# Optimization experiments

Measured on AMD Instinct MI355X. Metric: run time of the kernel, lower is better.

Reference implementation:

```python
import jax, jax.numpy as jnp
import numpy as np

H = 16
D_MODEL = 1024
D_K = D_MODEL // H


def setup_inputs() -> dict:
    key = jax.random.key(0)
    ks = jax.random.split(key, 12)
    B, S = 2, 2048
    scale = 1.0 / np.sqrt(D_MODEL)
    inp = {
        "query": jax.random.normal(ks[0], (B, S, D_MODEL), jnp.float32),
        "key": jax.random.normal(ks[1], (B, S, D_MODEL), jnp.float32),
        "value": jax.random.normal(ks[2], (B, S, D_MODEL), jnp.float32),
        "mask": jax.random.randint(ks[3], (B, S, S), 0, 2, jnp.int32),
        "w_q": jax.random.normal(ks[4], (D_MODEL, D_MODEL), jnp.float32) * scale,
        "b_q": jnp.zeros((D_MODEL,), jnp.float32),
        "w_k": jax.random.normal(ks[5], (D_MODEL, D_MODEL), jnp.float32) * scale,
        "b_k": jnp.zeros((D_MODEL,), jnp.float32),
        "w_v": jax.random.normal(ks[6], (D_MODEL, D_MODEL), jnp.float32) * scale,
        "b_v": jnp.zeros((D_MODEL,), jnp.float32),
        "w_o": jax.random.normal(ks[7], (D_MODEL, D_MODEL), jnp.float32) * scale,
        "b_o": jnp.zeros((D_MODEL,), jnp.float32),
    }
    return inp


def reference(query, key, value, mask, w_q, b_q, w_k, b_k, w_v, b_v, w_o, b_o):
    B, S, _ = query.shape
    # linear projections (torch nn.Linear: x @ W^T + b)
    q = query @ w_q.T + b_q
    k = key @ w_k.T + b_k
    v = value @ w_v.T + b_v
    # split heads -> [B, H, S, D_K]
    q = q.reshape(B, S, H, D_K).transpose(0, 2, 1, 3)
    k = k.reshape(B, S, H, D_K).transpose(0, 2, 1, 3)
    v = v.reshape(B, S, H, D_K).transpose(0, 2, 1, 3)
    # scores [B, H, S, S]; original masks BEFORE dividing by sqrt(d_k)
    scores = jnp.einsum("bhqd,bhkd->bhqk", q, k)
    m = mask[:, None, :, :]  # broadcast over heads (mask.unsqueeze(1))
    scores = jnp.where(m == 0, jnp.float32(-1e9), scores)
    scores = scores / jnp.sqrt(jnp.float32(D_K))
    attn = jax.nn.softmax(scores, axis=-1)
    # dropout is identity in eval mode
    ctx = jnp.einsum("bhqk,bhkd->bhqd", attn, v)
    ctx = ctx.transpose(0, 2, 1, 3).reshape(B, S, H * D_K)
    return ctx @ w_o.T + b_o
```

## Files before the change

kernel.cpp:

```cpp
#include <hip/hip_runtime.h>
#include <hip/hip_bf16.h>
#include <stdint.h>

typedef __attribute__((ext_vector_type(8))) short short8;
typedef __attribute__((ext_vector_type(4))) short short4v;
typedef __attribute__((ext_vector_type(4))) float f32x4;
typedef __attribute__((ext_vector_type(4))) unsigned short us4;
typedef unsigned short ushort_t;

#define LDS_AS __attribute__((address_space(3)))
#define GLB_AS __attribute__((address_space(1)))

__device__ __forceinline__ void gload_lds16(const void* g, void* l) {
    __builtin_amdgcn_global_load_lds((const GLB_AS uint32_t*)g, (LDS_AS uint32_t*)l, 16, 0, 0);
}

__device__ __forceinline__ unsigned short f2bf(float f) {
    union { float f; uint32_t u; } v; v.f = f;
    uint32_t r = v.u + 0x7FFFu + ((v.u >> 16) & 1u);
    return (unsigned short)(r >> 16);
}

__device__ __forceinline__ float fexp2(float x) {
#if __has_builtin(__builtin_amdgcn_exp2f)
    return __builtin_amdgcn_exp2f(x);
#else
    return exp2f(x);
#endif
}

__device__ __forceinline__ uint32_t fbits(float f) {
    union { float f; uint32_t u; } v; v.f = f; return v.u;
}

__device__ __forceinline__ f32x4 mfma32(short8 a, short8 b, f32x4 c) {
    return __builtin_amdgcn_mfma_f32_16x16x32_bf16(a, b, c, 0, 0, 0);
}
__device__ __forceinline__ f32x4 mfma16(short4v a, short4v b, f32x4 c) {
    return __builtin_amdgcn_mfma_f32_16x16x16bf16_1k(a, b, c, 0, 0, 0);
}

__device__ __forceinline__ short8 lds_frag(const char* base, int row, int kc) {
    int byte = row * 128 + ((kc ^ (row & 7)) << 4);
    return *(const short8*)(base + byte);
}

__global__ __launch_bounds__(256) void cvt_all(
    const float* p0, const float* p1, const float* p2, const float* p3,
    const float* p4, const float* p5, const float* p6,
    ushort_t* o0, ushort_t* o1, ushort_t* o2, ushort_t* o3,
    ushort_t* o4, ushort_t* o5, ushort_t* o6) {
    int z = blockIdx.y;
    const float* in = z == 0 ? p0 : z == 1 ? p1 : z == 2 ? p2 : z == 3 ? p3 : z == 4 ? p4 : z == 5 ? p5 : p6;
    ushort_t* out = z == 0 ? o0 : z == 1 ? o1 : z == 2 ? o2 : z == 3 ? o3 : z == 4 ? o4 : z == 5 ? o5 : o6;
    int n4 = z < 3 ? 1048576 : 262144;
    int i = blockIdx.x * 256 + threadIdx.x;
    int stride = gridDim.x * 256;
    for (; i < n4; i += stride) {
        float4 f = ((const float4*)in)[i];
        us4 o;
        o[0] = f2bf(f.x); o[1] = f2bf(f.y); o[2] = f2bf(f.z); o[3] = f2bf(f.w);
        ((us4*)out)[i] = o;
    }
}

__global__ __launch_bounds__(256) void pack_mask(const int* __restrict__ mask,
                                                 unsigned long long* __restrict__ out) {
    int i = blockIdx.x * 256 + threadIdx.x;
    unsigned long long bits = __ballot(mask[i] != 0);
    if ((threadIdx.x & 63) == 0) {
        int k = i & 2047, q = (i >> 11) & 2047, b = i >> 22;
        out[((size_t)b * 32 + (k >> 6)) * 2048 + q] = bits;
    }
}

template<int MI>
__device__ __forceinline__ void gemm_core(const ushort_t* Ab, const ushort_t* Wb,
                                          char* ldsA, char* ldsW, int tid, f32x4 acc[MI][4]) {
    constexpr int K = 1024;
    int lane = tid & 63, wid = tid >> 6;
    int cl = lane & 15, gr = lane >> 4;
    int wm = (wid >> 1) * (MI * 16), wn = (wid & 1) * 64;
#pragma unroll
    for (int i = 0; i < MI; ++i)
#pragma unroll
        for (int j = 0; j < 4; ++j) acc[i][j] = (f32x4)0.0f;

    for (int kt = 0; kt < K / 64; ++kt) {
        int k0 = kt * 64;
#pragma unroll
        for (int iss = 0; iss < MI; ++iss) {
            int c = iss * 256 + tid;
            int r = c >> 3, kc = (c & 7) ^ (r & 7);
            gload_lds16(Ab + (size_t)r * K + k0 + kc * 8, ldsA + c * 16);
        }
#pragma unroll
        for (int iss = 0; iss < 4; ++iss) {
            int c = iss * 256 + tid;
            int r = c >> 3, kc = (c & 7) ^ (r & 7);
            gload_lds16(Wb + (size_t)r * K + k0 + kc * 8, ldsW + c * 16);
        }
        __syncthreads();
#pragma unroll
        for (int ks = 0; ks < 2; ++ks) {
            short8 af[MI], wf[4];
#pragma unroll
            for (int t = 0; t < MI; ++t)
                af[t] = lds_frag(ldsA, wm + t * 16 + cl, ks * 4 + gr);
#pragma unroll
            for (int t = 0; t < 4; ++t)
                wf[t] = lds_frag(ldsW, wn + t * 16 + cl, ks * 4 + gr);
#pragma unroll
            for (int i = 0; i < MI; ++i)
#pragma unroll
                for (int j = 0; j < 4; ++j)
                    acc[i][j] = mfma32(af[i], wf[j], acc[i][j]);
        }
        __syncthreads();
    }
}

template<int MI>
__global__ __launch_bounds__(256, 4)
void gemm3(const ushort_t* A0, const ushort_t* A1, const ushort_t* A2,
           const ushort_t* W0, const ushort_t* W1, const ushort_t* W2,
           const float* B0, const float* B1, const float* B2,
           void* O0, void* O1, void* O2, int mode_ovr, float scl0) {
    __shared__ char lds[MI * 4096 + 16384];
    char* ldsA = lds;
    char* ldsW = lds + MI * 4096;

    int gx = gridDim.x, gy = gridDim.y;
    int nwg = gx * gy * gridDim.z;
    int bid = blockIdx.x + gx * (blockIdx.y + gy * blockIdx.z);
    int nb = (bid & 7) * (nwg >> 3) + (bid >> 3);
    int bx = nb % gx;
    int t2 = nb / gx;
    int by = t2 % gy;
    int z = t2 / gy;

    const ushort_t* A = z == 0 ? A0 : z == 1 ? A1 : A2;
    const ushort_t* W = z == 0 ? W0 : z == 1 ? W1 : W2;
    const float* bias = z == 0 ? B0 : z == 1 ? B1 : B2;
    void* out = z == 0 ? O0 : z == 1 ? O1 : O2;
    int mode = mode_ovr >= 0 ? mode_ovr : (z == 2 ? 1 : 0);
    float scl = z == 0 ? scl0 : 1.0f;

    int tid = threadIdx.x, lane = tid & 63, wid = tid >> 6;
    int cl = lane & 15, gr = lane >> 4;
    int wm = (wid >> 1) * (MI * 16), wn = (wid & 1) * 64;
    int bm = by * (MI * 32), bn = bx * 128;

    f32x4 acc[MI][4];
    gemm_core<MI>(A + (size_t)bm * 1024, W + (size_t)bn * 1024, ldsA, ldsW, tid, acc);

#pragma unroll
    for (int j = 0; j < 4; ++j) {
        int n = bn + wn + j * 16 + cl;
        float bv = bias[n];
#pragma unroll
        for (int i = 0; i < MI; ++i) {
            int mbase = bm + wm + i * 16 + gr * 4;
            if (mode == 0) {
#pragma unroll
                for (int r = 0; r < 4; ++r) {
                    int m = mbase + r;
                    float v = (acc[i][j][r] + bv) * scl;
                    size_t idx = (((size_t)((m >> 11) * 16 + (n >> 6))) * 2048 + (m & 2047)) * 64 + (n & 63);
                    ((ushort_t*)out)[idx] = f2bf(v);
                }
            } else if (mode == 1) {
                us4 pk;
#pragma unroll
                for (int r = 0; r < 4; ++r) pk[r] = f2bf(acc[i][j][r] + bv);
                size_t idx = (((size_t)((mbase >> 11) * 16 + (n >> 6))) * 64 + (n & 63)) * 2048 + (mbase & 2047);
                *(us4*)((ushort_t*)out + idx) = pk;
            } else {
#pragma unroll
                for (int r = 0; r < 4; ++r)
                    ((float*)out)[(size_t)(mbase + r) * 1024 + n] = acc[i][j][r] + bv;
            }
        }
    }
}

__global__ __launch_bounds__(512, 4)
void attn(const ushort_t* __restrict__ Q, const ushort_t* __restrict__ Kh,
          const ushort_t* __restrict__ Vt, const unsigned long long* __restrict__ PM,
          ushort_t* __restrict__ ctx) {
    constexpr int S = 2048;
    __shared__ char lds[65536];
    int tid = threadIdx.x, lane = tid & 63, wid = tid >> 6;
    int cl = lane & 15, gr = lane >> 4, c7 = cl & 7;
    int h2 = wid & 1;
    int qg = wid >> 1;

    int blk = (blockIdx.x & 7) * 64 + (blockIdx.x >> 3);
    int bh = blk >> 4, qt = blk & 15;
    int b = bh >> 4, h = bh & 15;
    const ushort_t* Qb = Q + (size_t)bh * S * 64;
    const ushort_t* Kb = Kh + (size_t)bh * S * 64;
    const ushort_t* Vb = Vt + (size_t)bh * 64 * S;
    int q0w = qt * 128 + qg * 32;

    short8 qreg[2][2];
#pragma unroll
    for (int qf = 0; qf < 2; ++qf)
#pragma unroll
        for (int ks = 0; ks < 2; ++ks)
            qreg[qf][ks] = *(const short8*)(Qb + (size_t)(q0w + qf * 16 + cl) * 64 + ks * 32 + gr * 8);

    f32x4 acc[2][4];
    f32x4 accl[2];
#pragma unroll
    for (int qf = 0; qf < 2; ++qf) {
        accl[qf] = (f32x4)0.0f;
#pragma unroll
        for (int df = 0; df < 4; ++df) acc[qf][df] = (f32x4)0.0f;
    }

    int hs = tid >> 8, stid = tid & 255;
    int kOff[2], vOff[2], dstL[2];
#pragma unroll
    for (int iss = 0; iss < 2; ++iss) {
        int L = iss * 256 + stid;
        int r = L >> 3, c = (L & 7) ^ (r & 7);
        kOff[iss] = r * 64 + c * 8;
        vOff[iss] = r * S + c * 8;
        dstL[iss] = L * 16;
    }
    char* sbase = lds + hs * 32768;

    int aK0 = cl * 128 + ((0 * 4 + gr) ^ c7) * 16;
    int aK1 = cl * 128 + ((1 * 4 + gr) ^ c7) * 16;
    int aV[4];
#pragma unroll
    for (int nf = 0; nf < 4; ++nf)
        aV[nf] = cl * 128 + (((2 * nf) + (gr >> 1)) ^ c7) * 16 + (gr & 1) * 8;

    const unsigned long long* pmq = PM + (size_t)b * 32 * 2048 + q0w + cl;

    short4v ones;
#pragma unroll
    for (int r = 0; r < 4; ++r) ones[r] = (short)0x3F80;

    auto stage = [&](int T, int parity) {
        const ushort_t* Ks = Kb + (size_t)T * 4096;
        const ushort_t* Vs = Vb + (size_t)T * 64;
        char* dst = sbase + parity * 16384;
#pragma unroll
        for (int iss = 0; iss < 2; ++iss) {
            gload_lds16(Ks + kOff[iss], dst + dstL[iss]);
            gload_lds16(Vs + vOff[iss], dst + 8192 + dstL[iss]);
        }
    };

    stage(hs * 16, 0);
    __syncthreads();

    char* mybase = lds + h2 * 32768;
    for (int t = 0; t < 16; ++t) {
        char* cb = mybase + (t & 1) * 16384;
        if (t < 15) stage(hs * 16 + t + 1, (t + 1) & 1);

        int kvi = h2 * 16 + t;
        unsigned long long w0 = pmq[(size_t)kvi * 2048];
        unsigned long long w1 = pmq[(size_t)kvi * 2048 + 16];

        f32x4 sc[2][4];
#pragma unroll
        for (int nf = 0; nf < 4; ++nf) {
            short8 k0 = *(const short8*)(cb + aK0 + nf * 2048);
            short8 k1 = *(const short8*)(cb + aK1 + nf * 2048);
#pragma unroll
            for (int qf = 0; qf < 2; ++qf) {
                f32x4 s = mfma32(k0, qreg[qf][0], (f32x4)0.0f);
                sc[qf][nf] = mfma32(k1, qreg[qf][1], s);
            }
        }

        short4v pk[2][4];
#pragma unroll
        for (int qf = 0; qf < 2; ++qf) {
            unsigned long long ws = (qf == 0 ? w0 : w1) >> (gr * 4);
            uint32_t lo = (uint32_t)ws, hi = (uint32_t)(ws >> 32);
#pragma unroll
            for (int nf = 0; nf < 4; ++nf) {
                uint32_t wb = nf < 2 ? lo : hi;
                uint32_t u[4];
#pragma unroll
                for (int r = 0; r < 4; ++r) {
                    uint32_t bit = wb & (1u << ((nf & 1) * 16 + r));
                    float sel = bit ? sc[qf][nf][r] : -1.0e9f;
                    u[r] = fbits(fexp2(sel)) + 0x8000u;
                }
                union { uint32_t d[2]; short4v v; } pp;
                pp.d[0] = __builtin_amdgcn_perm(u[1], u[0], 0x07060302u);
                pp.d[1] = __builtin_amdgcn_perm(u[3], u[2], 0x07060302u);
                pk[qf][nf] = pp.v;
            }
        }

#pragma unroll
        for (int nf = 0; nf < 4; ++nf) {
#pragma unroll
            for (int df = 0; df < 4; ++df) {
                short4v vf = *(const short4v*)(cb + 8192 + aV[nf] + df * 2048);
                acc[0][df] = mfma16(pk[0][nf], vf, acc[0][df]);
                acc[1][df] = mfma16(pk[1][nf], vf, acc[1][df]);
            }
            accl[0] = mfma16(pk[0][nf], ones, accl[0]);
            accl[1] = mfma16(pk[1][nf], ones, accl[1]);
        }
        __syncthreads();
    }

    if (h2) {
        float* dst = (float*)(lds + qg * 10240 + lane * 160);
#pragma unroll
        for (int qf = 0; qf < 2; ++qf) {
#pragma unroll
            for (int df = 0; df < 4; ++df)
                *(f32x4*)(dst + qf * 16 + df * 4) = acc[qf][df];
            *(f32x4*)(dst + 32 + qf * 4) = accl[qf];
        }
    }
    __syncthreads();
    if (!h2) {
        const float* src = (const float*)(lds + qg * 10240 + lane * 160);
#pragma unroll
        for (int qf = 0; qf < 2; ++qf) {
#pragma unroll
            for (int df = 0; df < 4; ++df)
                acc[qf][df] += *(const f32x4*)(src + qf * 16 + df * 4);
            accl[qf] += *(const f32x4*)(src + 32 + qf * 4);
        }
#pragma unroll
        for (int qf = 0; qf < 2; ++qf) {
            float inv[4];
#pragma unroll
            for (int r = 0; r < 4; ++r) inv[r] = 1.0f / accl[qf][r];
#pragma unroll
            for (int df = 0; df < 4; ++df)
#pragma unroll
                for (int r = 0; r < 4; ++r) {
                    int q = q0w + qf * 16 + gr * 4 + r;
                    int d = df * 16 + cl;
                    ctx[((size_t)b * S + q) * 1024 + h * 64 + d] = f2bf(acc[qf][df][r] * inv[r]);
                }
        }
    }
}

extern "C" void kernel_launch(void* const* d_in, const int* in_sizes, int n_in,
                              void* d_out, int out_size, void* d_ws, size_t ws_size,
                              hipStream_t stream) {
    const float* query = (const float*)d_in[0];
    const float* key   = (const float*)d_in[1];
    const float* value = (const float*)d_in[2];
    const int*   mask  = (const int*)d_in[3];
    const float* w_q = (const float*)d_in[4];
    const float* b_q = (const float*)d_in[5];
    const float* w_k = (const float*)d_in[6];
    const float* b_k = (const float*)d_in[7];
    const float* w_v = (const float*)d_in[8];
    const float* b_v = (const float*)d_in[9];
    const float* w_o = (const float*)d_in[10];
    const float* b_o = (const float*)d_in[11];

    char* ws = (char*)d_ws;
    const size_t MB = 1 << 20;
    ushort_t* xq  = (ushort_t*)(ws + 0 * MB);
    ushort_t* xk  = (ushort_t*)(ws + 8 * MB);
    ushort_t* xv  = (ushort_t*)(ws + 16 * MB);
    ushort_t* wq  = (ushort_t*)(ws + 24 * MB);
    ushort_t* wk  = (ushort_t*)(ws + 26 * MB);
    ushort_t* wv  = (ushort_t*)(ws + 28 * MB);
    ushort_t* wo  = (ushort_t*)(ws + 30 * MB);
    ushort_t* qhm = (ushort_t*)(ws + 32 * MB);
    ushort_t* khm = (ushort_t*)(ws + 40 * MB);
    ushort_t* vt  = (ushort_t*)(ws + 48 * MB);
    unsigned long long* pm = (unsigned long long*)(ws + 56 * MB);
    ushort_t* ctx = (ushort_t*)(ws + 0 * MB);

    const float QSCALE = 0.125f * 1.44269504088896f;

    cvt_all<<<dim3(1024, 7), 256, 0, stream>>>(query, key, value, w_q, w_k, w_v, w_o,
                                               xq, xk, xv, wq, wk, wv, wo);
    pack_mask<<<32768, 256, 0, stream>>>(mask, pm);

    gemm3<2><<<dim3(8, 64, 3), 256, 0, stream>>>(xq, xk, xv, wq, wk, wv, b_q, b_k, b_v,
                                                 qhm, khm, vt, -1, QSCALE);

    attn<<<512, 512, 0, stream>>>(qhm, khm, vt, pm, ctx);

    gemm3<2><<<dim3(8, 64, 1), 256, 0, stream>>>(ctx, ctx, ctx, wo, wo, wo, b_o, b_o, b_o,
                                                 d_out, d_out, d_out, 2, 1.0f);
}
```

Before: 150.3 us.

## Double-buffer LDS tiles in projection GEMM to overlap loads with MFMA

The projection GEMM core now keeps two LDS tile buffers. It issues the async global-to-LDS loads for the next K-slice before running MFMAs on the current one, which removes the barrier that used to sit between load and compute in every iteration. Per-thread load offsets are precomputed once outside the loop. LDS use doubles, and the launch-bounds occupancy hint drops from 4 to 3 blocks per CU, so fewer waves are resident to hide latency.

```diff
diff --git a/kernel.cpp b/kernel.cpp
--- a/kernel.cpp
+++ b/kernel.cpp
@@ -76,8 +76,10 @@
 
 template<int MI>
 __device__ __forceinline__ void gemm_core(const ushort_t* Ab, const ushort_t* Wb,
-                                          char* ldsA, char* ldsW, int tid, f32x4 acc[MI][4]) {
+                                          char* lds, int tid, f32x4 acc[MI][4]) {
     constexpr int K = 1024;
+    constexpr int ABYTES = MI * 4096;
+    constexpr int TILE = ABYTES + 16384;
     int lane = tid & 63, wid = tid >> 6;
     int cl = lane & 15, gr = lane >> 4;
     int wm = (wid >> 1) * (MI * 16), wn = (wid & 1) * 64;
@@ -86,30 +88,49 @@
 #pragma unroll
         for (int j = 0; j < 4; ++j) acc[i][j] = (f32x4)0.0f;
 
+    int aOff[MI], aDst[MI], bOff[4], bDst[4];
+#pragma unroll
+    for (int iss = 0; iss < MI; ++iss) {
+        int c = iss * 256 + tid;
+        int r = c >> 3, kc = (c & 7) ^ (r & 7);
+        aOff[iss] = r * K + kc * 8;
+        aDst[iss] = c * 16;
+    }
+#pragma unroll
+    for (int iss = 0; iss < 4; ++iss) {
+        int c = iss * 256 + tid;
+        int r = c >> 3, kc = (c & 7) ^ (r & 7);
+        bOff[iss] = r * K + kc * 8;
+        bDst[iss] = c * 16;
+    }
+
+    auto stage = [&](int kt, char* dst) {
+        int k0 = kt * 64;
+#pragma unroll
+        for (int iss = 0; iss < MI; ++iss)
+            gload_lds16(Ab + aOff[iss] + k0, dst + aDst[iss]);
+#pragma unroll
+        for (int iss = 0; iss < 4; ++iss)
+            gload_lds16(Wb + bOff[iss] + k0, dst + ABYTES + bDst[iss]);
+    };
+
+    stage(0, lds);
+    __syncthreads();
+
     for (int kt = 0; kt < K / 64; ++kt) {
-        int k0 = kt * 64;
-#pragma unroll
-        for (int iss = 0; iss < MI; ++iss) {
-            int c = iss * 256 + tid;
-            int r = c >> 3, kc = (c & 7) ^ (r & 7);
-            gload_lds16(Ab + (size_t)r * K + k0 + kc * 8, ldsA + c * 16);
-        }
-#pragma unroll
-        for (int iss = 0; iss < 4; ++iss) {
-            int c = iss * 256 + tid;
-            int r = c >> 3, kc = (c & 7) ^ (r & 7);
-            gload_lds16(Wb + (size_t)r * K + k0 + kc * 8, ldsW + c * 16);
-        }
-        __syncthreads();
+        char* cb = lds + (kt & 1) * TILE;
+        if (kt < K / 64 - 1) stage(kt + 1, lds + ((kt + 1) & 1) * TILE);
+        char* cA = cb;
+        char* cW = cb + ABYTES;
 #pragma unroll
         for (int ks = 0; ks < 2; ++ks) {
             short8 af[MI], wf[4];
 #pragma unroll
             for (int t = 0; t < MI; ++t)
-                af[t] = lds_frag(ldsA, wm + t * 16 + cl, ks * 4 + gr);
+                af[t] = lds_frag(cA, wm + t * 16 + cl, ks * 4 + gr);
 #pragma unroll
             for (int t = 0; t < 4; ++t)
-                wf[t] = lds_frag(ldsW, wn + t * 16 + cl, ks * 4 + gr);
+                wf[t] = lds_frag(cW, wn + t * 16 + cl, ks * 4 + gr);
 #pragma unroll
             for (int i = 0; i < MI; ++i)
 #pragma unroll
@@ -121,14 +142,12 @@
 }
 
 template<int MI>
-__global__ __launch_bounds__(256, 4)
+__global__ __launch_bounds__(256, 3)
 void gemm3(const ushort_t* A0, const ushort_t* A1, const ushort_t* A2,
            const ushort_t* W0, const ushort_t* W1, const ushort_t* W2,
            const float* B0, const float* B1, const float* B2,
            void* O0, void* O1, void* O2, int mode_ovr, float scl0) {
-    __shared__ char lds[MI * 4096 + 16384];
-    char* ldsA = lds;
-    char* ldsW = lds + MI * 4096;
+    __shared__ char lds[2 * (MI * 4096 + 16384)];
 
     int gx = gridDim.x, gy = gridDim.y;
     int nwg = gx * gy * gridDim.z;
@@ -152,7 +171,7 @@
     int bm = by * (MI * 32), bn = bx * 128;
 
     f32x4 acc[MI][4];
-    gemm_core<MI>(A + (size_t)bm * 1024, W + (size_t)bn * 1024, ldsA, ldsW, tid, acc);
+    gemm_core<MI>(A + (size_t)bm * 1024, W + (size_t)bn * 1024, lds, tid, acc);
 
 #pragma unroll
     for (int j = 0; j < 4; ++j) {
```

After: 144.8 us. 1.04x faster.
